# Performance work log

Measured on AMD Instinct MI355X. Metric: run time of the kernel, lower is better.

Reference implementation:

```python
import jax, jax.numpy as jnp
import numpy as np

B, S, E, H = 4, 2048, 1024, 16
D = E // H
LR_MULT = 100.0
EPS = 1e-5

def setup_inputs() -> dict:
    key = jax.random.key(0)
    ks = jax.random.split(key, 4)
    x = jax.random.normal(ks[0], (B, S, E), dtype=jnp.float32)
    # nn.MultiheadAttention in_proj_weight [3E,E], out_proj.weight [E,E] (bias=False)
    W_qkv = jax.random.normal(ks[1], (3 * E, E), dtype=jnp.float32) * (1.0 / np.sqrt(E))
    W_o = jax.random.normal(ks[2], (E, E), dtype=jnp.float32) * (1.0 / np.sqrt(E))
    ln_w = jnp.ones((E,), dtype=jnp.float32)
    scaler = jnp.asarray(1.0 / LR_MULT, dtype=jnp.float32)
    return {"x": x, "W_qkv": W_qkv, "W_o": W_o, "ln_w": ln_w, "scaler": scaler}

def _layernorm(x, w):
    mu = jnp.mean(x, axis=-1, keepdims=True)
    var = jnp.mean(jnp.square(x - mu), axis=-1, keepdims=True)
    return (x - mu) * jax.lax.rsqrt(var + EPS) * w

def reference(x, W_qkv, W_o, ln_w, scaler):
    resid = x
    xn = _layernorm(x, ln_w)
    qkv = jnp.einsum('bse,fe->bsf', xn, W_qkv)  # [B,S,3E]
    q, k, v = jnp.split(qkv, 3, axis=-1)
    q = q.reshape(B, S, H, D)
    k = k.reshape(B, S, H, D)
    v = v.reshape(B, S, H, D)
    scores = jnp.einsum('bihd,bjhd->bhij', q, k) / jnp.sqrt(jnp.asarray(D, x.dtype))
    # linear_encoding_base[i,j] = j - i; bias = softplus(100*scaler)*(j-i) where j<=i else -inf
    i_idx = jnp.arange(S)
    rel = (i_idx[None, :] - i_idx[:, None]).astype(x.dtype)  # j - i
    causal = i_idx[None, :] <= i_idx[:, None]                # tril: j <= i
    slope = jax.nn.softplus(LR_MULT * scaler)
    bias = jnp.where(causal, slope * rel, -jnp.inf)          # [S,S]
    att = jax.nn.softmax(scores + bias[None, None, :, :], axis=-1)
    out = jnp.einsum('bhij,bjhd->bihd', att, v).reshape(B, S, E)
    out = jnp.einsum('bse,fe->bsf', out, W_o)
    return out + resid
```

## Files before the change

### kernel.cpp

```cpp
#include <hip/hip_runtime.h>

typedef unsigned short u16;
typedef unsigned int u32;
typedef __bf16 bf16x8 __attribute__((ext_vector_type(8)));
typedef float f32x4 __attribute__((ext_vector_type(4)));

#define B_ 4
#define S_ 2048
#define E_ 1024
#define H_ 16
#define D_ 64

__device__ __forceinline__ u16 f2bf(float f) {
  u32 u = __float_as_uint(f);
  u32 r = u + 0x7fffu + ((u >> 16) & 1u);
  return (u16)(r >> 16);
}

__global__ __launch_bounds__(256) void ln_kernel(const float* __restrict__ x,
                                                 const float* __restrict__ w,
                                                 u16* __restrict__ xn) {
  const int lane = threadIdx.x & 63;
  const int wv = threadIdx.x >> 6;
  const int row = blockIdx.x * 4 + wv;
  const float4* xr = (const float4*)(x + (size_t)row * E_);
  float4 vv[4];
  float s = 0.f, sq = 0.f;
#pragma unroll
  for (int i = 0; i < 4; ++i) {
    vv[i] = xr[lane + i * 64];
    s += vv[i].x + vv[i].y + vv[i].z + vv[i].w;
    sq += vv[i].x * vv[i].x + vv[i].y * vv[i].y + vv[i].z * vv[i].z + vv[i].w * vv[i].w;
  }
#pragma unroll
  for (int off = 1; off < 64; off <<= 1) {
    s += __shfl_xor(s, off);
    sq += __shfl_xor(sq, off);
  }
  const float mu = s * (1.f / E_);
  const float rs = rsqrtf(sq * (1.f / E_) - mu * mu + 1e-5f);
  u16* xo = xn + (size_t)row * E_;
  const float4* wr = (const float4*)w;
#pragma unroll
  for (int i = 0; i < 4; ++i) {
    float4 w4 = wr[lane + i * 64];
    ushort4 o;
    o.x = f2bf((vv[i].x - mu) * rs * w4.x);
    o.y = f2bf((vv[i].y - mu) * rs * w4.y);
    o.z = f2bf((vv[i].z - mu) * rs * w4.z);
    o.w = f2bf((vv[i].w - mu) * rs * w4.w);
    ((ushort4*)xo)[lane + i * 64] = o;
  }
}

__global__ __launch_bounds__(256) void cvt_kernel(const float* __restrict__ src,
                                                  u16* __restrict__ dst) {
  const int i = blockIdx.x * 256 + threadIdx.x;
  float4 v = ((const float4*)src)[i];
  ushort4 o;
  o.x = f2bf(v.x);
  o.y = f2bf(v.y);
  o.z = f2bf(v.z);
  o.w = f2bf(v.w);
  ((ushort4*)dst)[i] = o;
}

template <int EPI>
__global__ __launch_bounds__(256) void gemm_bt(const u16* __restrict__ A,
                                               const u16* __restrict__ Bw,
                                               const int K,
                                               u16* __restrict__ qo, u16* __restrict__ ko,
                                               u16* __restrict__ vo,
                                               const float* __restrict__ xres,
                                               float* __restrict__ outp) {
  __shared__ u16 As[128 * 72];
  __shared__ u16 Bs[128 * 72];
  const int t = threadIdx.x;
  const int lane = t & 63, wv = t >> 6;
  const int wm = wv >> 1, wn = wv & 1;
  const int m0 = blockIdx.y * 128, n0 = blockIdx.x * 128;
  const int r16 = lane & 15, g4 = lane >> 4;

  const f32x4 fzero = {0.f, 0.f, 0.f, 0.f};
  f32x4 acc[4][4];
#pragma unroll
  for (int i = 0; i < 4; ++i)
#pragma unroll
    for (int j = 0; j < 4; ++j) acc[i][j] = fzero;

  const int srow = t >> 3;
  const int scol = (t & 7) * 8;

  for (int kt = 0; kt < K; kt += 64) {
    uint4 va[4], vb[4];
#pragma unroll
    for (int i = 0; i < 4; ++i) {
      const int row = srow + i * 32;
      va[i] = *(const uint4*)(A + (size_t)(m0 + row) * K + kt + scol);
      vb[i] = *(const uint4*)(Bw + (size_t)(n0 + row) * K + kt + scol);
    }
#pragma unroll
    for (int i = 0; i < 4; ++i) {
      const int row = srow + i * 32;
      *(uint4*)&As[row * 72 + scol] = va[i];
      *(uint4*)&Bs[row * 72 + scol] = vb[i];
    }
    __syncthreads();
    bf16x8 af[4][2], bf2[4][2];
#pragma unroll
    for (int mi = 0; mi < 4; ++mi)
#pragma unroll
      for (int kc = 0; kc < 2; ++kc)
        af[mi][kc] = *(const bf16x8*)&As[(wm * 64 + mi * 16 + r16) * 72 + kc * 32 + g4 * 8];
#pragma unroll
    for (int ni = 0; ni < 4; ++ni)
#pragma unroll
      for (int kc = 0; kc < 2; ++kc)
        bf2[ni][kc] = *(const bf16x8*)&Bs[(wn * 64 + ni * 16 + r16) * 72 + kc * 32 + g4 * 8];
#pragma unroll
    for (int mi = 0; mi < 4; ++mi)
#pragma unroll
      for (int ni = 0; ni < 4; ++ni)
#pragma unroll
        for (int kc = 0; kc < 2; ++kc)
          acc[mi][ni] = __builtin_amdgcn_mfma_f32_16x16x32_bf16(af[mi][kc], bf2[ni][kc],
                                                                acc[mi][ni], 0, 0, 0);
    __syncthreads();
  }

  if constexpr (EPI == 0) {
#pragma unroll
    for (int mi = 0; mi < 4; ++mi)
#pragma unroll
      for (int e = 0; e < 4; ++e) {
        const int gr = m0 + wm * 64 + mi * 16 + g4 * 4 + e;
        const int bb = gr >> 11, ss = gr & 2047;
#pragma unroll
        for (int ni = 0; ni < 4; ++ni) {
          const int gc = n0 + wn * 64 + ni * 16 + r16;
          const int which = gc >> 10;
          const int hh = (gc >> 6) & 15;
          const int dd = gc & 63;
          u16* dst = which == 0 ? qo : (which == 1 ? ko : vo);
          dst[(((size_t)bb * H_ + hh) * S_ + ss) * D_ + dd] = f2bf(acc[mi][ni][e]);
        }
      }
  } else {
#pragma unroll
    for (int mi = 0; mi < 4; ++mi)
#pragma unroll
      for (int e = 0; e < 4; ++e) {
        const int gr = m0 + wm * 64 + mi * 16 + g4 * 4 + e;
#pragma unroll
        for (int ni = 0; ni < 4; ++ni) {
          const int gc = n0 + wn * 64 + ni * 16 + r16;
          const size_t idx = (size_t)gr * 1024 + gc;
          outp[idx] = acc[mi][ni][e] + xres[idx];
        }
      }
  }
}

__global__ __launch_bounds__(256) void attn_kernel(const u16* __restrict__ q,
                                                   const u16* __restrict__ k,
                                                   const u16* __restrict__ v,
                                                   const float* __restrict__ scaler_p,
                                                   u16* __restrict__ ao) {
  __shared__ u16 Qs[64 * 72];
  __shared__ u16 Ks[64 * 72];
  __shared__ u16 Vt[64 * 72];
  __shared__ u16 Ps[4 * 16 * 72];
  const int t = threadIdx.x;
  const int lane = t & 63, wv = t >> 6;
  const int r16 = lane & 15, g4 = lane >> 4;
  const int it = blockIdx.x;
  const int bh = blockIdx.y;
  const int bb = bh >> 4, hh = bh & 15;
  const size_t base = (size_t)bh * (S_ * D_);

  const float tt = 100.f * scaler_p[0];
  const float slope = (tt > 20.f) ? tt : log1pf(expf(tt));
  const float L2E = 1.4426950408889634f;
  const float qs_l2e = 0.125f * L2E;
  const float sl_l2e = slope * L2E;
  int nb = (int)ceilf(80.f / (slope * 64.f));
  if (nb < 1) nb = 1;
  int jt0 = it - nb;
  if (jt0 < 0) jt0 = 0;

  {
    const int r = t >> 2, c = (t & 3) << 4;
    const u16* gp = q + base + (size_t)(it * 64 + r) * D_ + c;
    uint4 a0 = ((const uint4*)gp)[0];
    uint4 a1 = ((const uint4*)gp)[1];
    *(uint4*)&Qs[r * 72 + c] = a0;
    *(uint4*)&Qs[r * 72 + c + 8] = a1;
  }

  float mrun[4] = {-3e38f, -3e38f, -3e38f, -3e38f};
  float lrun[4] = {0.f, 0.f, 0.f, 0.f};
  const f32x4 fzero = {0.f, 0.f, 0.f, 0.f};
  f32x4 oacc[4];
#pragma unroll
  for (int i = 0; i < 4; ++i) oacc[i] = fzero;

  bf16x8 qa[2];
  bool qloaded = false;

  for (int jt = jt0; jt <= it; ++jt) {
    {
      const int r = t >> 2, c = (t & 3) << 4;
      const u16* kg = k + base + (size_t)(jt * 64 + r) * D_ + c;
      uint4 k0 = ((const uint4*)kg)[0];
      uint4 k1 = ((const uint4*)kg)[1];
      *(uint4*)&Ks[r * 72 + c] = k0;
      *(uint4*)&Ks[r * 72 + c + 8] = k1;
      const u16* vg = v + base + (size_t)(jt * 64 + r) * D_ + c;
      union { uint4 u; u16 s[8]; } v0, v1;
      v0.u = ((const uint4*)vg)[0];
      v1.u = ((const uint4*)vg)[1];
#pragma unroll
      for (int j = 0; j < 8; ++j) {
        Vt[(c + j) * 72 + r] = v0.s[j];
        Vt[(c + 8 + j) * 72 + r] = v1.s[j];
      }
    }
    __syncthreads();
    if (!qloaded) {
      qloaded = true;
#pragma unroll
      for (int kc = 0; kc < 2; ++kc)
        qa[kc] = *(const bf16x8*)&Qs[(wv * 16 + r16) * 72 + kc * 32 + g4 * 8];
    }
    f32x4 sfr[4];
#pragma unroll
    for (int nt = 0; nt < 4; ++nt) {
      sfr[nt] = fzero;
#pragma unroll
      for (int kc = 0; kc < 2; ++kc) {
        bf16x8 kb = *(const bf16x8*)&Ks[(nt * 16 + r16) * 72 + kc * 32 + g4 * 8];
        sfr[nt] = __builtin_amdgcn_mfma_f32_16x16x32_bf16(qa[kc], kb, sfr[nt], 0, 0, 0);
      }
    }
    const bool diag = (jt == it);
    const float jb = (float)((jt - it) * 64);
    float pm[4] = {-3e38f, -3e38f, -3e38f, -3e38f};
#pragma unroll
    for (int nt = 0; nt < 4; ++nt) {
      const int jl = nt * 16 + r16;
#pragma unroll
      for (int e = 0; e < 4; ++e) {
        const int il = wv * 16 + g4 * 4 + e;
        float sc = sfr[nt][e] * qs_l2e + sl_l2e * (jb + (float)(jl - il));
        if (diag && jl > il) sc = -3e38f;
        sfr[nt][e] = sc;
        pm[e] = fmaxf(pm[e], sc);
      }
    }
#pragma unroll
    for (int e = 0; e < 4; ++e) {
#pragma unroll
      for (int off = 1; off < 16; off <<= 1) pm[e] = fmaxf(pm[e], __shfl_xor(pm[e], off));
    }
    u16* Psw = Ps + wv * (16 * 72);
    float psum[4] = {0.f, 0.f, 0.f, 0.f};
#pragma unroll
    for (int e = 0; e < 4; ++e) {
      const float mn = fmaxf(mrun[e], pm[e]);
      const float rsc = exp2f(mrun[e] - mn);
      mrun[e] = mn;
      lrun[e] *= rsc;
#pragma unroll
      for (int nt = 0; nt < 4; ++nt) oacc[nt][e] *= rsc;
    }
#pragma unroll
    for (int nt = 0; nt < 4; ++nt)
#pragma unroll
      for (int e = 0; e < 4; ++e) {
        const float p = exp2f(sfr[nt][e] - mrun[e]);
        psum[e] += p;
        Psw[(g4 * 4 + e) * 72 + nt * 16 + r16] = f2bf(p);
      }
#pragma unroll
    for (int e = 0; e < 4; ++e) {
#pragma unroll
      for (int off = 1; off < 16; off <<= 1) psum[e] += __shfl_xor(psum[e], off);
      lrun[e] += psum[e];
    }
    bf16x8 pa[2];
#pragma unroll
    for (int jk = 0; jk < 2; ++jk)
      pa[jk] = *(const bf16x8*)&Psw[r16 * 72 + jk * 32 + g4 * 8];
#pragma unroll
    for (int nt = 0; nt < 4; ++nt)
#pragma unroll
      for (int jk = 0; jk < 2; ++jk) {
        bf16x8 vb = *(const bf16x8*)&Vt[(nt * 16 + r16) * 72 + jk * 32 + g4 * 8];
        oacc[nt] = __builtin_amdgcn_mfma_f32_16x16x32_bf16(pa[jk], vb, oacc[nt], 0, 0, 0);
      }
    __syncthreads();
  }
#pragma unroll
  for (int e = 0; e < 4; ++e) {
    const float inv = 1.f / lrun[e];
    const int row = it * 64 + wv * 16 + g4 * 4 + e;
#pragma unroll
    for (int nt = 0; nt < 4; ++nt) {
      const int col = hh * 64 + nt * 16 + r16;
      ao[((size_t)bb * S_ + row) * E_ + col] = f2bf(oacc[nt][e] * inv);
    }
  }
}

extern "C" void kernel_launch(void* const* d_in, const int* in_sizes, int n_in,
                              void* d_out, int out_size, void* d_ws, size_t ws_size,
                              hipStream_t stream) {
  const float* x = (const float*)d_in[0];
  const float* Wqkv = (const float*)d_in[1];
  const float* Wo = (const float*)d_in[2];
  const float* lnw = (const float*)d_in[3];
  const float* scaler = (const float*)d_in[4];
  float* out = (float*)d_out;
  char* ws = (char*)d_ws;

  u16* xn = (u16*)(ws + 0);
  u16* q = (u16*)(ws + 16777216);
  u16* kk = (u16*)(ws + 33554432);
  u16* vv = (u16*)(ws + 50331648);
  u16* ao = (u16*)(ws + 67108864);
  u16* wqkvb = (u16*)(ws + 83886080);
  u16* wob = (u16*)(ws + 90177536);

  ln_kernel<<<2048, 256, 0, stream>>>(x, lnw, xn);
  cvt_kernel<<<3072, 256, 0, stream>>>(Wqkv, wqkvb);
  cvt_kernel<<<1024, 256, 0, stream>>>(Wo, wob);
  gemm_bt<0><<<dim3(24, 64), 256, 0, stream>>>(xn, wqkvb, 1024, q, kk, vv, nullptr, nullptr);
  attn_kernel<<<dim3(32, 64), 256, 0, stream>>>(q, kk, vv, scaler, ao);
  gemm_bt<1><<<dim3(8, 64), 256, 0, stream>>>(ao, wob, 1024, nullptr, nullptr, nullptr, x, out);
}
```

Before: 152.2 us.

## Double-buffer GEMM tiles with direct global-to-LDS async loads

The projection GEMM now stages A and B tiles straight from global memory into LDS with global_load_lds, into two ping-pong buffers. The next K tile is loaded while the current one is being multiplied, which removes the register round-trip and one barrier per iteration. Because of the direct-load layout, the LDS rows are no longer padded, so the 16-byte fragment reads may hit more bank conflicts. It also requests two blocks per CU through launch bounds and hoists the q/k/v destination choice out of the epilogue loop.

```diff
diff --git a/kernel.cpp b/kernel.cpp
--- a/kernel.cpp
+++ b/kernel.cpp
@@ -15,6 +15,11 @@
   u32 u = __float_as_uint(f);
   u32 r = u + 0x7fffu + ((u >> 16) & 1u);
   return (u16)(r >> 16);
+}
+
+__device__ __forceinline__ void gload16(const u16* g, u16* l) {
+  __builtin_amdgcn_global_load_lds((const __attribute__((address_space(1))) void*)g,
+                                   (__attribute__((address_space(3))) void*)l, 16, 0, 0);
 }
 
 __global__ __launch_bounds__(256) void ln_kernel(const float* __restrict__ x,
@@ -66,15 +71,14 @@
 }
 
 template <int EPI>
-__global__ __launch_bounds__(256) void gemm_bt(const u16* __restrict__ A,
-                                               const u16* __restrict__ Bw,
-                                               const int K,
-                                               u16* __restrict__ qo, u16* __restrict__ ko,
-                                               u16* __restrict__ vo,
-                                               const float* __restrict__ xres,
-                                               float* __restrict__ outp) {
-  __shared__ u16 As[128 * 72];
-  __shared__ u16 Bs[128 * 72];
+__global__ __launch_bounds__(256, 2) void gemm_bt(const u16* __restrict__ A,
+                                                  const u16* __restrict__ Bw,
+                                                  const int K,
+                                                  u16* __restrict__ qo, u16* __restrict__ ko,
+                                                  u16* __restrict__ vo,
+                                                  const float* __restrict__ xres,
+                                                  float* __restrict__ outp) {
+  __shared__ u16 lds[2][2][128 * 64];
   const int t = threadIdx.x;
   const int lane = t & 63, wv = t >> 6;
   const int wm = wv >> 1, wn = wv & 1;
@@ -88,47 +92,57 @@
 #pragma unroll
     for (int j = 0; j < 4; ++j) acc[i][j] = fzero;
 
-  const int srow = t >> 3;
-  const int scol = (t & 7) * 8;
-
-  for (int kt = 0; kt < K; kt += 64) {
-    uint4 va[4], vb[4];
+  const int srow8 = lane >> 3;
+  const int scol = (lane & 7) * 8;
+
+  auto stage = [&](int bu, int kt) {
 #pragma unroll
     for (int i = 0; i < 4; ++i) {
-      const int row = srow + i * 32;
-      va[i] = *(const uint4*)(A + (size_t)(m0 + row) * K + kt + scol);
-      vb[i] = *(const uint4*)(Bw + (size_t)(n0 + row) * K + kt + scol);
-    }
-#pragma unroll
-    for (int i = 0; i < 4; ++i) {
-      const int row = srow + i * 32;
-      *(uint4*)&As[row * 72 + scol] = va[i];
-      *(uint4*)&Bs[row * 72 + scol] = vb[i];
-    }
+      const int c = wv * 4 + i;
+      const int row = c * 8 + srow8;
+      gload16(A + (size_t)(m0 + row) * K + kt + scol, &lds[bu][0][c * 512]);
+      gload16(Bw + (size_t)(n0 + row) * K + kt + scol, &lds[bu][1][c * 512]);
+    }
+  };
+
+  auto compute = [&](int bu) {
+    const u16* As = lds[bu][0];
+    const u16* Bs = lds[bu][1];
+    bf16x8 af[4][2], bfr[4][2];
+#pragma unroll
+    for (int mi = 0; mi < 4; ++mi)
+#pragma unroll
+      for (int kc = 0; kc < 2; ++kc)
+        af[mi][kc] = *(const bf16x8*)&As[(wm * 64 + mi * 16 + r16) * 64 + kc * 32 + g4 * 8];
+#pragma unroll
+    for (int ni = 0; ni < 4; ++ni)
+#pragma unroll
+      for (int kc = 0; kc < 2; ++kc)
+        bfr[ni][kc] = *(const bf16x8*)&Bs[(wn * 64 + ni * 16 + r16) * 64 + kc * 32 + g4 * 8];
+#pragma unroll
+    for (int mi = 0; mi < 4; ++mi)
+#pragma unroll
+      for (int ni = 0; ni < 4; ++ni)
+#pragma unroll
+        for (int kc = 0; kc < 2; ++kc)
+          acc[mi][ni] = __builtin_amdgcn_mfma_f32_16x16x32_bf16(af[mi][kc], bfr[ni][kc],
+                                                                acc[mi][ni], 0, 0, 0);
+  };
+
+  stage(0, 0);
+  __syncthreads();
+  int cur = 0;
+  for (int kt = 64; kt < K; kt += 64) {
+    stage(cur ^ 1, kt);
+    compute(cur);
     __syncthreads();
-    bf16x8 af[4][2], bf2[4][2];
-#pragma unroll
-    for (int mi = 0; mi < 4; ++mi)
-#pragma unroll
-      for (int kc = 0; kc < 2; ++kc)
-        af[mi][kc] = *(const bf16x8*)&As[(wm * 64 + mi * 16 + r16) * 72 + kc * 32 + g4 * 8];
-#pragma unroll
-    for (int ni = 0; ni < 4; ++ni)
-#pragma unroll
-      for (int kc = 0; kc < 2; ++kc)
-        bf2[ni][kc] = *(const bf16x8*)&Bs[(wn * 64 + ni * 16 + r16) * 72 + kc * 32 + g4 * 8];
-#pragma unroll
-    for (int mi = 0; mi < 4; ++mi)
-#pragma unroll
-      for (int ni = 0; ni < 4; ++ni)
-#pragma unroll
-        for (int kc = 0; kc < 2; ++kc)
-          acc[mi][ni] = __builtin_amdgcn_mfma_f32_16x16x32_bf16(af[mi][kc], bf2[ni][kc],
-                                                                acc[mi][ni], 0, 0, 0);
-    __syncthreads();
-  }
+    cur ^= 1;
+  }
+  compute(cur);
 
   if constexpr (EPI == 0) {
+    const int which = n0 >> 10;
+    u16* dst = which == 0 ? qo : (which == 1 ? ko : vo);
 #pragma unroll
     for (int mi = 0; mi < 4; ++mi)
 #pragma unroll
@@ -138,10 +152,8 @@
 #pragma unroll
         for (int ni = 0; ni < 4; ++ni) {
           const int gc = n0 + wn * 64 + ni * 16 + r16;
-          const int which = gc >> 10;
           const int hh = (gc >> 6) & 15;
           const int dd = gc & 63;
-          u16* dst = which == 0 ? qo : (which == 1 ? ko : vo);
           dst[(((size_t)bb * H_ + hh) * S_ + ss) * D_ + dd] = f2bf(acc[mi][ni][e]);
         }
       }
```

Result: faster. 141.5 us (-7.1%).
